# Kernel optimization log

Measured on AMD Instinct MI355X. Metric: run time of the kernel, lower is better.

Reference implementation:

```python
import math
import jax, jax.numpy as jnp
import numpy as np

INP_MODES = [4, 8, 8, 4]   # prod = 1024 = in_features
OUT_MODES = [8, 8, 8, 8]   # prod = 4096 = out_features
TT_RANKS = [1, 8, 8, 8, 1]
IN_FEATURES = 1024
OUT_FEATURES = 4096
BATCH = 8192
D = len(INP_MODES)


def setup_inputs() -> dict:
    key = jax.random.key(0)
    ks = jax.random.split(key, D + 2)
    inp = {"x": jax.random.normal(ks[0], (BATCH, IN_FEATURES), dtype=jnp.float32)}
    for i in range(D):
        # xavier_normal per the module's reset_parameters
        fan_in = TT_RANKS[i] * INP_MODES[i]
        fan_out = TT_RANKS[i + 1] * OUT_MODES[i]
        std = math.sqrt(2.0 / (fan_in + fan_out))
        shape = (TT_RANKS[i] * OUT_MODES[i], TT_RANKS[i + 1] * INP_MODES[i])
        inp[f"core{i}"] = std * jax.random.normal(ks[i + 1], shape, dtype=jnp.float32)
    bound = 1.0 / math.sqrt(IN_FEATURES)
    inp["bias"] = jax.random.uniform(ks[D + 1], (OUT_FEATURES,), dtype=jnp.float32,
                                     minval=-bound, maxval=bound)
    return inp


def _tt_forward(x, cores, bias):
    # x: [B, in_features]. Sequentially contract input modes against TT cores.
    # Invariant after step i: h has shape (B, M=prod(m_0..m_i), r_{i+1}, N=prod(n_{i+1}..))
    B = x.shape[0]
    h = x.reshape(B, 1, 1, IN_FEATURES)
    for i, c in enumerate(cores):
        r, m, q, n = TT_RANKS[i], OUT_MODES[i], TT_RANKS[i + 1], INP_MODES[i]
        c4 = c.reshape(r, m, q, n)          # (r_i, m_i, r_{i+1}, n_i)
        M = h.shape[1]
        h = h.reshape(B, M, r, n, -1)       # split current input mode n_i
        # contract rank r_i and input mode n_i; produce out mode m_i (s) and next rank q
        h = jnp.einsum('bmrnp,rsqn->bmsqp', h, c4)
        h = h.reshape(B, M * m, q, -1)
    y = h.reshape(B, OUT_FEATURES) + bias
    return y


def reference(x, core0, core1, core2, core3, bias):
    return _tt_forward(x, [core0, core1, core2, core3], bias)
```

## Files before the change

### kernel.cpp

```cpp
#include <hip/hip_runtime.h>
#include <hip/hip_bf16.h>

typedef __bf16 bf16x4 __attribute__((ext_vector_type(4)));
typedef __bf16 bf16x8 __attribute__((ext_vector_type(8)));
typedef float  f32x4  __attribute__((ext_vector_type(4)));
typedef float  f32x16 __attribute__((ext_vector_type(16)));

#define MFMA32(a,b,c) __builtin_amdgcn_mfma_f32_32x32x16_bf16((a),(b),(c),0,0,0)

#define BAR_LDS() asm volatile("s_waitcnt lgkmcnt(0)\n\ts_barrier" ::: "memory")


__global__ __launch_bounds__(256) void tt_kernel(
    const float* __restrict__ x,  const float* __restrict__ c0,
    const float* __restrict__ c1, const float* __restrict__ c2,
    const float* __restrict__ c3, const float* __restrict__ bias,
    float* __restrict__ y)
{
    __shared__ __align__(16) __bf16 w23l[16384];
    __shared__ __align__(16) __bf16 xt[2048];
    __shared__ __align__(16) __bf16 hb[16384];

    const int tid  = threadIdx.x;
    const int wid  = tid >> 6;
    const int lane = tid & 63;
    const int hh   = lane >> 5;
    const int c32  = lane & 31;
    const int rt   = wid & 1;
    const int ct   = wid >> 1;

    {
      const int r = tid >> 2, kb = (tid & 3) * 64;
      const int m2 = r >> 3, m3 = r & 7;
      float c3v[8][4];
      #pragma unroll
      for (int r3 = 0; r3 < 8; ++r3)
        #pragma unroll
        for (int n3 = 0; n3 < 4; ++n3)
          c3v[r3][n3] = c3[(r3 * 8 + m3) * 4 + n3];
      for (int j = 0; j < 64; ++j) {
        const int k = kb + j;
        const int n2 = k >> 5, n3 = (k >> 3) & 3, r2 = k & 7;
        float s = 0.f;
        #pragma unroll
        for (int r3 = 0; r3 < 8; ++r3)
          s += c2[(r2 * 8 + m2) * 64 + r3 * 8 + n2] * c3v[r3][n3];
        w23l[r * 256 + (((k >> 3) ^ (r & 31)) << 3) + (k & 7)] = (__bf16)s;
      }
    }

    bf16x8 w01f[8][2];
    {
      const int row = rt * 32 + c32, m1 = row >> 3, r2w = row & 7;
      float c1row[8][8];
      #pragma unroll
      for (int r1 = 0; r1 < 8; ++r1)
        #pragma unroll
        for (int n1 = 0; n1 < 8; ++n1)
          c1row[r1][n1] = c1[(r1 * 8 + m1) * 64 + r2w * 8 + n1];
      for (int m0 = 0; m0 < 8; ++m0) {
        #pragma unroll
        for (int kt = 0; kt < 2; ++kt) {
          const int n0 = kt * 2 + hh;
          #pragma unroll
          for (int j = 0; j < 8; ++j) {
            float s = 0.f;
            #pragma unroll
            for (int r1 = 0; r1 < 8; ++r1)
              s += c0[m0 * 32 + r1 * 4 + n0] * c1row[r1][j];
            w01f[m0][kt][j] = (__bf16)s;
          }
        }
      }
    }

    float bv[2][4][4];
    #pragma unroll
    for (int q = 0; q < 2; ++q)
      #pragma unroll
      for (int p = 0; p < 4; ++p)
        #pragma unroll
        for (int i = 0; i < 4; ++i)
          bv[q][p][i] = bias[q * 2048 + p * 512 + (hh * 4 + i) * 64 + rt * 32 + c32];

    const int bsel = tid >> 7, xcol = tid & 31, k0q = (tid >> 5) & 3;
    const int xtoff = (bsel * 32 + xcol) * 32 + ((k0q ^ (xcol & 3)) << 3);

    float xv[8];
    {
      const float* xp = x + (size_t)(blockIdx.x * 16 + bsel) * 1024 + xcol;
      #pragma unroll
      for (int j = 0; j < 8; ++j) xv[j] = xp[(k0q * 8 + j) * 32];
      bf16x8 v;
      #pragma unroll
      for (int j = 0; j < 8; ++j) v[j] = (__bf16)xv[j];
      *(bf16x8*)&xt[xtoff] = v;
    }
    BAR_LDS();

    for (int it = 0; it < 8; ++it) {
      const int b0 = (blockIdx.x * 8 + it) * 2;

      bf16x8 xf[2];
      #pragma unroll
      for (int kt = 0; kt < 2; ++kt)
        xf[kt] = *(const bf16x8*)
          &xt[(ct * 32 + c32) * 32 + (((kt * 2 + hh) ^ (c32 & 3)) << 3)];

      #pragma unroll
      for (int q = 0; q < 2; ++q) {
        if (q == 0) {
          const int itn = (it + 1) & 7;
          const float* xp = x + (size_t)((blockIdx.x * 8 + itn) * 2 + bsel) * 1024 + xcol;
          #pragma unroll
          for (int j = 0; j < 8; ++j) xv[j] = xp[(k0q * 8 + j) * 32];
        }

        #pragma unroll
        for (int m0h = 0; m0h < 4; ++m0h) {
          f32x16 acc = {};
          acc = MFMA32(w01f[q * 4 + m0h][0], xf[0], acc);
          acc = MFMA32(w01f[q * 4 + m0h][1], xf[1], acc);
          #pragma unroll
          for (int p = 0; p < 4; ++p) {
            bf16x4 o;
            #pragma unroll
            for (int i = 0; i < 4; ++i) o[i] = (__bf16)acc[p * 4 + i];
            const int cl = ct * 32 + m0h * 8 + rt * 4 + p;
            *(bf16x4*)&hb[cl * 256 + ((c32 ^ (cl & 31)) << 3) + hh * 4] = o;
          }
        }
        BAR_LDS();

        const __bf16* arow = &w23l[(rt * 32 + c32) * 256];
        const __bf16* brow = &hb[(ct * 32 + c32) * 256];
        f32x16 acc2a = {}, acc2b = {};
        #pragma unroll
        for (int kt = 0; kt < 16; kt += 2) {
          const int op0 = ((kt * 2 + hh) ^ c32) << 3;
          const int op1 = ((kt * 2 + 2 + hh) ^ c32) << 3;
          acc2a = MFMA32(*(const bf16x8*)&brow[op0], *(const bf16x8*)&arow[op0], acc2a);
          acc2b = MFMA32(*(const bf16x8*)&brow[op1], *(const bf16x8*)&arow[op1], acc2b);
        }

        if (q == 1) {
          bf16x8 v;
          #pragma unroll
          for (int j = 0; j < 8; ++j) v[j] = (__bf16)xv[j];
          *(bf16x8*)&xt[xtoff] = v;
        }

        {
          const size_t ybase = (size_t)(b0 + ct) * 4096 + q * 2048 + rt * 32 + c32;
          #pragma unroll
          for (int p = 0; p < 4; ++p)
            #pragma unroll
            for (int i = 0; i < 4; ++i)
              y[ybase + p * 512 + (hh * 4 + i) * 64] =
                  (acc2a[p * 4 + i] + acc2b[p * 4 + i]) + bv[q][p][i];
        }
        BAR_LDS();
      }
    }
}

extern "C" void kernel_launch(void* const* d_in, const int* in_sizes, int n_in,
                              void* d_out, int out_size, void* d_ws, size_t ws_size,
                              hipStream_t stream) {
    const float* x    = (const float*)d_in[0];
    const float* c0   = (const float*)d_in[1];
    const float* c1   = (const float*)d_in[2];
    const float* c2   = (const float*)d_in[3];
    const float* c3   = (const float*)d_in[4];
    const float* bias = (const float*)d_in[5];
    float* yout = (float*)d_out;
    tt_kernel<<<512, 256, 0, stream>>>(x, c0, c1, c2, c3, bias, yout);
}
```

Measured before the change: 210.8 us.

## Double-buffer hidden and x tiles, keep W23 in registers, software-pipeline stages

Moves the W23 factor from LDS into per-wave registers, loaded once after the precompute. This frees LDS so the hidden-state and x tiles can be double-buffered. The main loop is restructured so stage A of the next half-tile overlaps stage B and the epilogue of the current one, halving the barriers per iteration. It also sets launch bounds for 2 blocks per CU. The cost is higher register pressure from 16 bf16x8 W23 fragments, which the occupancy hint may force into spills.

After: 287.7 us. +36.5%, slower.

```diff
diff --git a/kernel.cpp b/kernel.cpp
--- a/kernel.cpp
+++ b/kernel.cpp
@@ -11,15 +11,14 @@
 #define BAR_LDS() asm volatile("s_waitcnt lgkmcnt(0)\n\ts_barrier" ::: "memory")
 
 
-__global__ __launch_bounds__(256) void tt_kernel(
+__global__ __launch_bounds__(256, 2) void tt_kernel(
     const float* __restrict__ x,  const float* __restrict__ c0,
     const float* __restrict__ c1, const float* __restrict__ c2,
     const float* __restrict__ c3, const float* __restrict__ bias,
     float* __restrict__ y)
 {
-    __shared__ __align__(16) __bf16 w23l[16384];
-    __shared__ __align__(16) __bf16 xt[2048];
-    __shared__ __align__(16) __bf16 hb[16384];
+    __shared__ __align__(16) __bf16 hb[2][16384];
+    __shared__ __align__(16) __bf16 xt[2][2048];
 
     const int tid  = threadIdx.x;
     const int wid  = tid >> 6;
@@ -28,6 +27,69 @@
     const int c32  = lane & 31;
     const int rt   = wid & 1;
     const int ct   = wid >> 1;
+
+    const int bsel = tid >> 7, xcol = tid & 31, k0q = (tid >> 5) & 3;
+    const int xtoff = (bsel * 32 + xcol) * 32 + ((k0q ^ (xcol & 3)) << 3);
+
+#define LOAD_X(itn) do { \
+    const float* xp_ = x + (size_t)((blockIdx.x * 8 + (itn)) * 2 + bsel) * 1024 + xcol; \
+    _Pragma("unroll") \
+    for (int j = 0; j < 8; ++j) xv[j] = xp_[(k0q * 8 + j) * 32]; \
+  } while (0)
+
+#define WRITE_XT(itb) do { \
+    bf16x8 v_; \
+    _Pragma("unroll") \
+    for (int j = 0; j < 8; ++j) v_[j] = (__bf16)xv[j]; \
+    *(bf16x8*)&xt[itb][xtoff] = v_; \
+  } while (0)
+
+#define READ_XF(itb) do { \
+    _Pragma("unroll") \
+    for (int kt = 0; kt < 2; ++kt) \
+      xf[kt] = *(const bf16x8*) \
+        &xt[itb][(ct * 32 + c32) * 32 + (((kt * 2 + hh) ^ (c32 & 3)) << 3)]; \
+  } while (0)
+
+#define STAGE_A(qc, buf) do { \
+    _Pragma("unroll") \
+    for (int m0h = 0; m0h < 4; ++m0h) { \
+      f32x16 acc_ = {}; \
+      acc_ = MFMA32(w01f[(qc) * 4 + m0h][0], xf[0], acc_); \
+      acc_ = MFMA32(w01f[(qc) * 4 + m0h][1], xf[1], acc_); \
+      _Pragma("unroll") \
+      for (int p = 0; p < 4; ++p) { \
+        bf16x4 o_; \
+        _Pragma("unroll") \
+        for (int i = 0; i < 4; ++i) o_[i] = (__bf16)acc_[p * 4 + i]; \
+        const int cl_ = ct * 32 + m0h * 8 + rt * 4 + p; \
+        *(bf16x4*)&hb[buf][cl_ * 256 + ((c32 ^ (cl_ & 31)) << 3) + hh * 4] = o_; \
+      } \
+    } \
+  } while (0)
+
+#define STAGE_B_EPI(qc, buf, itp) do { \
+    const __bf16* brow_ = &hb[buf][(ct * 32 + c32) * 256]; \
+    f32x16 a2a_ = {}, a2b_ = {}; \
+    _Pragma("unroll") \
+    for (int kt = 0; kt < 16; kt += 2) { \
+      const int op0_ = ((kt * 2 + hh) ^ c32) << 3; \
+      const int op1_ = ((kt * 2 + 2 + hh) ^ c32) << 3; \
+      a2a_ = MFMA32(*(const bf16x8*)&brow_[op0_], w23f[kt], a2a_); \
+      a2b_ = MFMA32(*(const bf16x8*)&brow_[op1_], w23f[kt + 1], a2b_); \
+    } \
+    const size_t yb_ = (size_t)((blockIdx.x * 8 + (itp)) * 2 + ct) * 4096 \
+                       + (qc) * 2048 + rt * 32 + c32; \
+    _Pragma("unroll") \
+    for (int p = 0; p < 4; ++p) \
+      _Pragma("unroll") \
+      for (int i = 0; i < 4; ++i) \
+        y[yb_ + p * 512 + (hh * 4 + i) * 64] = \
+            (a2a_[p * 4 + i] + a2b_[p * 4 + i]) + bv[qc][p][i]; \
+  } while (0)
+
+    float xv[8];
+    LOAD_X(0);
 
     {
       const int r = tid >> 2, kb = (tid & 3) * 64;
@@ -45,7 +107,7 @@
         #pragma unroll
         for (int r3 = 0; r3 < 8; ++r3)
           s += c2[(r2 * 8 + m2) * 64 + r3 * 8 + n2] * c3v[r3][n3];
-        w23l[r * 256 + (((k >> 3) ^ (r & 31)) << 3) + (k & 7)] = (__bf16)s;
+        hb[1][r * 256 + (((k >> 3) ^ (r & 31)) << 3) + (k & 7)] = (__bf16)s;
       }
     }
 
@@ -83,85 +145,44 @@
         for (int i = 0; i < 4; ++i)
           bv[q][p][i] = bias[q * 2048 + p * 512 + (hh * 4 + i) * 64 + rt * 32 + c32];
 
-    const int bsel = tid >> 7, xcol = tid & 31, k0q = (tid >> 5) & 3;
-    const int xtoff = (bsel * 32 + xcol) * 32 + ((k0q ^ (xcol & 3)) << 3);
-
-    float xv[8];
-    {
-      const float* xp = x + (size_t)(blockIdx.x * 16 + bsel) * 1024 + xcol;
-      #pragma unroll
-      for (int j = 0; j < 8; ++j) xv[j] = xp[(k0q * 8 + j) * 32];
-      bf16x8 v;
-      #pragma unroll
-      for (int j = 0; j < 8; ++j) v[j] = (__bf16)xv[j];
-      *(bf16x8*)&xt[xtoff] = v;
-    }
+    WRITE_XT(0);
     BAR_LDS();
 
-    for (int it = 0; it < 8; ++it) {
-      const int b0 = (blockIdx.x * 8 + it) * 2;
+    bf16x8 w23f[16];
+    {
+      const __bf16* wrow = &hb[1][(rt * 32 + c32) * 256];
+      #pragma unroll
+      for (int kt = 0; kt < 16; ++kt)
+        w23f[kt] = *(const bf16x8*)&wrow[((kt * 2 + hh) ^ c32) << 3];
+    }
+    bf16x8 xf[2];
+    READ_XF(0);
+    LOAD_X(1);
+    STAGE_A(0, 0);
+    BAR_LDS();
 
-      bf16x8 xf[2];
-      #pragma unroll
-      for (int kt = 0; kt < 2; ++kt)
-        xf[kt] = *(const bf16x8*)
-          &xt[(ct * 32 + c32) * 32 + (((kt * 2 + hh) ^ (c32 & 3)) << 3)];
+    #pragma unroll 1
+    for (int it = 0; it < 7; ++it) {
+      STAGE_A(1, 1);
+      STAGE_B_EPI(0, 0, it);
+      WRITE_XT((it + 1) & 1);
+      BAR_LDS();
+      READ_XF((it + 1) & 1);
+      if (it < 6) LOAD_X(it + 2);
+      STAGE_A(0, 0);
+      STAGE_B_EPI(1, 1, it);
+      BAR_LDS();
+    }
+    STAGE_A(1, 1);
+    STAGE_B_EPI(0, 0, 7);
+    BAR_LDS();
+    STAGE_B_EPI(1, 1, 7);
 
-      #pragma unroll
-      for (int q = 0; q < 2; ++q) {
-        if (q == 0) {
-          const int itn = (it + 1) & 7;
-          const float* xp = x + (size_t)((blockIdx.x * 8 + itn) * 2 + bsel) * 1024 + xcol;
-          #pragma unroll
-          for (int j = 0; j < 8; ++j) xv[j] = xp[(k0q * 8 + j) * 32];
-        }
-
-        #pragma unroll
-        for (int m0h = 0; m0h < 4; ++m0h) {
-          f32x16 acc = {};
-          acc = MFMA32(w01f[q * 4 + m0h][0], xf[0], acc);
-          acc = MFMA32(w01f[q * 4 + m0h][1], xf[1], acc);
-          #pragma unroll
-          for (int p = 0; p < 4; ++p) {
-            bf16x4 o;
-            #pragma unroll
-            for (int i = 0; i < 4; ++i) o[i] = (__bf16)acc[p * 4 + i];
-            const int cl = ct * 32 + m0h * 8 + rt * 4 + p;
-            *(bf16x4*)&hb[cl * 256 + ((c32 ^ (cl & 31)) << 3) + hh * 4] = o;
-          }
-        }
-        BAR_LDS();
-
-        const __bf16* arow = &w23l[(rt * 32 + c32) * 256];
-        const __bf16* brow = &hb[(ct * 32 + c32) * 256];
-        f32x16 acc2a = {}, acc2b = {};
-        #pragma unroll
-        for (int kt = 0; kt < 16; kt += 2) {
-          const int op0 = ((kt * 2 + hh) ^ c32) << 3;
-          const int op1 = ((kt * 2 + 2 + hh) ^ c32) << 3;
-          acc2a = MFMA32(*(const bf16x8*)&brow[op0], *(const bf16x8*)&arow[op0], acc2a);
-          acc2b = MFMA32(*(const bf16x8*)&brow[op1], *(const bf16x8*)&arow[op1], acc2b);
-        }
-
-        if (q == 1) {
-          bf16x8 v;
-          #pragma unroll
-          for (int j = 0; j < 8; ++j) v[j] = (__bf16)xv[j];
-          *(bf16x8*)&xt[xtoff] = v;
-        }
-
-        {
-          const size_t ybase = (size_t)(b0 + ct) * 4096 + q * 2048 + rt * 32 + c32;
-          #pragma unroll
-          for (int p = 0; p < 4; ++p)
-            #pragma unroll
-            for (int i = 0; i < 4; ++i)
-              y[ybase + p * 512 + (hh * 4 + i) * 64] =
-                  (acc2a[p * 4 + i] + acc2b[p * 4 + i]) + bv[q][p][i];
-        }
-        BAR_LDS();
-      }
-    }
+#undef LOAD_X
+#undef WRITE_XT
+#undef READ_XF
+#undef STAGE_A
+#undef STAGE_B_EPI
 }
 
 extern "C" void kernel_launch(void* const* d_in, const int* in_sizes, int n_in,
```
